# Optimization experiments

Hardware: AMD Instinct MI355X
Metric: run time of the kernel (lower is better)

The kernel has to match this reference:

```python
import jax, jax.numpy as jnp
import numpy as np

B, L, D = 64, 1024, 64  # (batch*heads, seq_len, head_dim)


def setup_inputs() -> dict:
    key = jax.random.key(0)
    kq, kk, kv = jax.random.split(key, 3)
    q = jax.random.normal(kq, (B, L, D), dtype=jnp.float32)
    k = jax.random.normal(kk, (B, L, D), dtype=jnp.float32)
    v = jax.random.normal(kv, (B, L, D), dtype=jnp.float32)
    scale = jnp.float32(1.0 / np.sqrt(D))  # standard 1/sqrt(d_head)
    return {"q": q, "k": k, "v": v, "scale": scale}


def reference(q, k, v, scale):
    # attention = bmm(q, k^T) * scale  -> [B, L, L]
    attention = jnp.einsum("bqd,bkd->bqk", q, k) * scale
    # softmax over dim=2 (keys); dropout p=0.0 is identity
    attention = jax.nn.softmax(attention, axis=2)
    # context = bmm(attention, v) -> [B, L, D]
    context = jnp.einsum("bqk,bkd->bqd", attention, v)
    return (context, attention)
```

## Files before the change

### kernel.cpp

```cpp
#include <hip/hip_runtime.h>
#include <hip/hip_bf16.h>

typedef __bf16 bf16x8 __attribute__((ext_vector_type(8)));
typedef float  f32x4  __attribute__((ext_vector_type(4)));

#define NB 64
#define LL 1024
#define DD 64
#define PSTR 36

#define LDS_K_BYTES (LL * DD * 2)
#define LDS_TOTAL   (LDS_K_BYTES + 8 * 16 * PSTR * 4)

__global__ __launch_bounds__(256)
void preconvert_v(const float* __restrict__ v, __bf16* __restrict__ vt) {
  const int blk = blockIdx.x, tid = threadIdx.x;
  const int b = blk >> 4, t = blk & 15;
  __shared__ float tile[64][65];
  const float* src = v + ((size_t)b * LL + t * 64) * DD;
  for (int i = tid; i < 64 * 16; i += 256) {
    const int row = i >> 4, c4 = (i & 15) * 4;
    f32x4 x = *(const f32x4*)(src + row * DD + c4);
    tile[row][c4 + 0] = x[0]; tile[row][c4 + 1] = x[1];
    tile[row][c4 + 2] = x[2]; tile[row][c4 + 3] = x[3];
  }
  __syncthreads();
  __bf16* dst = vt + (size_t)b * DD * LL + t * 64;
  for (int i = tid; i < 64 * 8; i += 256) {
    const int d = i >> 3, k8 = (i & 7) * 8;
    bf16x8 o;
    #pragma unroll
    for (int j = 0; j < 8; ++j) o[j] = (__bf16)tile[k8 + j][d];
    *(bf16x8*)(dst + (size_t)d * LL + k8) = o;
  }
}

__global__ __launch_bounds__(512, 1)
void sdpa_resident(const float* __restrict__ q, const float* __restrict__ kf,
                   const __bf16* __restrict__ vt, const float* __restrict__ scale_p,
                   float* __restrict__ out) {
  extern __shared__ char smem[];
  __bf16* Klds = (__bf16*)smem;
  float*  Pw   = (float*)(smem + LDS_K_BYTES);

  const int tid  = threadIdx.x;
  const int lane = tid & 63;
  const int w    = tid >> 6;
  const int l15  = lane & 15;
  const int lg   = lane >> 4;

  int bid = blockIdx.x;
  bid = (bid & 7) * 32 + (bid >> 3);
  const int b     = bid >> 2;
  const int qrow0 = (bid & 3) * 256 + w * 32;

  const float scale = scale_p[0];
  const float* kb = kf + (size_t)b * LL * DD;
  const __bf16* vb = vt + (size_t)b * DD * LL;
  float* ctxb  = out + ((size_t)b * LL + qrow0) * DD;
  float* attnb = out + (size_t)NB * LL * DD + (size_t)b * LL * LL
               + (size_t)qrow0 * LL;

  #pragma unroll
  for (int it = 0; it < 16; ++it) {
    const int c = it * 512 + tid;
    const int row = c >> 3, slot = c & 7;
    const f32x4* s4 = (const f32x4*)(kb + (size_t)c * 8);
    f32x4 x0 = s4[0], x1 = s4[1];
    bf16x8 t;
    #pragma unroll
    for (int j = 0; j < 4; ++j) { t[j] = (__bf16)x0[j]; t[4 + j] = (__bf16)x1[j]; }
    *(bf16x8*)(Klds + row * 64 + ((slot * 8) ^ ((row & 7) * 8))) = t;
  }

  bf16x8 aq[2][2];
  #pragma unroll
  for (int u = 0; u < 2; ++u) {
    const float* qrow = q + ((size_t)b * LL + qrow0 + u * 16 + l15) * DD;
    #pragma unroll
    for (int s = 0; s < 2; ++s) {
      const f32x4* p4 = (const f32x4*)(qrow + s * 32 + lg * 8);
      f32x4 x0 = p4[0], x1 = p4[1];
      #pragma unroll
      for (int j = 0; j < 4; ++j) {
        aq[u][s][j]     = (__bf16)(x0[j] * scale);
        aq[u][s][4 + j] = (__bf16)(x1[j] * scale);
      }
    }
  }

  __syncthreads();

  const int xsw = (l15 & 7) * 8;

  float lsum[2] = {0.f, 0.f};
  for (int kt = 0; kt < LL / 32; ++kt) {
    bf16x8 bk[2][2];
    #pragma unroll
    for (int f = 0; f < 2; ++f)
      #pragma unroll
      for (int s = 0; s < 2; ++s)
        bk[f][s] = *(const bf16x8*)(Klds + (kt * 32 + f * 16 + l15) * 64
                                         + ((s * 32 + lg * 8) ^ xsw));
    #pragma unroll
    for (int u = 0; u < 2; ++u) {
      f32x4 sacc[2] = {{0.f,0.f,0.f,0.f},{0.f,0.f,0.f,0.f}};
      #pragma unroll
      for (int s = 0; s < 2; ++s)
        #pragma unroll
        for (int f = 0; f < 2; ++f)
          sacc[f] = __builtin_amdgcn_mfma_f32_16x16x32_bf16(bk[f][s], aq[u][s], sacc[f], 0, 0, 0);
      #pragma unroll
      for (int f = 0; f < 2; ++f)
        #pragma unroll
        for (int r = 0; r < 4; ++r)
          lsum[u] += __expf(sacc[f][r]);
    }
  }
  #pragma unroll
  for (int u = 0; u < 2; ++u) {
    lsum[u] += __shfl_xor(lsum[u], 16, 64);
    lsum[u] += __shfl_xor(lsum[u], 32, 64);
  }
  const float rl[2] = {1.0f / lsum[0], 1.0f / lsum[1]};

  f32x4 cacc[2][4];
  #pragma unroll
  for (int u = 0; u < 2; ++u)
    #pragma unroll
    for (int g = 0; g < 4; ++g)
      cacc[u][g] = (f32x4){0.f, 0.f, 0.f, 0.f};

  float* prow = Pw + (w * 16 + l15) * PSTR;

  bf16x8 bvn[4];
  #pragma unroll
  for (int g = 0; g < 4; ++g)
    bvn[g] = *(const bf16x8*)(vb + (size_t)(g * 16 + l15) * LL + lg * 8);

  for (int kt = 0; kt < LL / 32; ++kt) {
    bf16x8 bvc[4];
    #pragma unroll
    for (int g = 0; g < 4; ++g) bvc[g] = bvn[g];
    if (kt + 1 < LL / 32) {
      #pragma unroll
      for (int g = 0; g < 4; ++g)
        bvn[g] = *(const bf16x8*)(vb + (size_t)(g * 16 + l15) * LL
                                     + (kt + 1) * 32 + lg * 8);
    }

    bf16x8 bk[2][2];
    #pragma unroll
    for (int f = 0; f < 2; ++f)
      #pragma unroll
      for (int s = 0; s < 2; ++s)
        bk[f][s] = *(const bf16x8*)(Klds + (kt * 32 + f * 16 + l15) * 64
                                         + ((s * 32 + lg * 8) ^ xsw));

    #pragma unroll
    for (int u = 0; u < 2; ++u) {
      f32x4 sacc[2] = {{0.f,0.f,0.f,0.f},{0.f,0.f,0.f,0.f}};
      #pragma unroll
      for (int s = 0; s < 2; ++s)
        #pragma unroll
        for (int f = 0; f < 2; ++f)
          sacc[f] = __builtin_amdgcn_mfma_f32_16x16x32_bf16(bk[f][s], aq[u][s], sacc[f], 0, 0, 0);

      f32x4 pv[2];
      #pragma unroll
      for (int f = 0; f < 2; ++f)
        #pragma unroll
        for (int r = 0; r < 4; ++r)
          pv[f][r] = __expf(sacc[f][r]) * rl[u];

      float* arow = attnb + (size_t)(u * 16 + l15) * LL + kt * 32 + lg * 4;
      *(f32x4*)(arow)      = pv[0];
      *(f32x4*)(arow + 16) = pv[1];

      *(f32x4*)(prow + lg * 4)      = pv[0];
      *(f32x4*)(prow + 16 + lg * 4) = pv[1];
      f32x4 p0 = *(const f32x4*)(prow + lg * 8);
      f32x4 p1 = *(const f32x4*)(prow + lg * 8 + 4);
      bf16x8 pa;
      #pragma unroll
      for (int j = 0; j < 4; ++j) { pa[j] = (__bf16)p0[j]; pa[4 + j] = (__bf16)p1[j]; }

      #pragma unroll
      for (int g = 0; g < 4; ++g)
        cacc[u][g] = __builtin_amdgcn_mfma_f32_16x16x32_bf16(pa, bvc[g], cacc[u][g], 0, 0, 0);
    }
  }

  #pragma unroll
  for (int u = 0; u < 2; ++u)
    #pragma unroll
    for (int g = 0; g < 4; ++g)
      #pragma unroll
      for (int r = 0; r < 4; ++r)
        ctxb[(size_t)(u * 16 + lg * 4 + r) * DD + g * 16 + l15] = cacc[u][g][r];
}

#define BQ 64
#define BK 32
#define KSTRIDE 72
#define VSTRIDE 40
#define PSTRIDE 48

__global__ __launch_bounds__(256, 4)
void sdpa_fallback(const float* __restrict__ q, const float* __restrict__ k,
                   const float* __restrict__ v, const float* __restrict__ scale_p,
                   float* __restrict__ out) {
  const int tid  = threadIdx.x;
  const int lane = tid & 63;
  const int w    = tid >> 6;
  int bid = blockIdx.x;
  bid = (bid & 7) * 128 + (bid >> 3);
  const int b    = bid >> 4;
  const int qblk = (bid & 15) * BQ;

  __shared__ __bf16 Ks[BK * KSTRIDE];
  __shared__ __bf16 Vs[DD * VSTRIDE];
  __shared__ __bf16 Pp[4][16 * PSTRIDE];

  const float scale = scale_p[0];
  const float* qb = q + ((size_t)b * LL + qblk) * DD;
  const float* kb = k + (size_t)b * LL * DD;
  const float* vb = v + (size_t)b * LL * DD;
  float* ctx  = out + ((size_t)b * LL + qblk) * DD;
  float* attn = out + (size_t)NB * LL * DD + (size_t)b * LL * LL + (size_t)qblk * LL;

  const int l15 = lane & 15;
  const int lg  = lane >> 4;
  const int dchunk = lg * 8;

  bf16x8 aq[2];
  {
    const float* qrow = qb + (size_t)(w * 16 + l15) * DD;
    #pragma unroll
    for (int s = 0; s < 2; ++s) {
      const f32x4* p4 = (const f32x4*)(qrow + s * 32 + dchunk);
      f32x4 x0 = p4[0], x1 = p4[1];
      #pragma unroll
      for (int j = 0; j < 4; ++j) {
        aq[s][j]     = (__bf16)(x0[j] * scale);
        aq[s][4 + j] = (__bf16)(x1[j] * scale);
      }
    }
  }

  const int srow = tid >> 3;
  const int sd0  = (tid & 7) * 8;

  float lpart[4] = {0.f, 0.f, 0.f, 0.f};
  for (int kt = 0; kt < LL / BK; ++kt) {
    __syncthreads();
    {
      const f32x4* src = (const f32x4*)(kb + (size_t)(kt * BK + srow) * DD + sd0);
      f32x4 x0 = src[0], x1 = src[1];
      bf16x8 t;
      #pragma unroll
      for (int j = 0; j < 4; ++j) { t[j] = (__bf16)x0[j]; t[4 + j] = (__bf16)x1[j]; }
      *(bf16x8*)&Ks[srow * KSTRIDE + sd0] = t;
    }
    __syncthreads();
    f32x4 sacc[2] = {{0.f,0.f,0.f,0.f},{0.f,0.f,0.f,0.f}};
    #pragma unroll
    for (int s = 0; s < 2; ++s)
      #pragma unroll
      for (int f = 0; f < 2; ++f) {
        bf16x8 bk = *(const bf16x8*)&Ks[(f * 16 + l15) * KSTRIDE + s * 32 + dchunk];
        sacc[f] = __builtin_amdgcn_mfma_f32_16x16x32_bf16(aq[s], bk, sacc[f], 0, 0, 0);
      }
    #pragma unroll
    for (int f = 0; f < 2; ++f)
      #pragma unroll
      for (int r = 0; r < 4; ++r)
        lpart[r] += __expf(sacc[f][r]);
  }
  #pragma unroll
  for (int m = 1; m < 16; m <<= 1)
    #pragma unroll
    for (int r = 0; r < 4; ++r)
      lpart[r] += __shfl_xor(lpart[r], m, 64);
  float rl[4];
  #pragma unroll
  for (int r = 0; r < 4; ++r) rl[r] = 1.0f / lpart[r];

  f32x4 cacc[4] = {{0.f,0.f,0.f,0.f},{0.f,0.f,0.f,0.f},
                   {0.f,0.f,0.f,0.f},{0.f,0.f,0.f,0.f}};
  for (int kt = 0; kt < LL / BK; ++kt) {
    __syncthreads();
    {
      const f32x4* src = (const f32x4*)(kb + (size_t)(kt * BK + srow) * DD + sd0);
      f32x4 x0 = src[0], x1 = src[1];
      bf16x8 t;
      #pragma unroll
      for (int j = 0; j < 4; ++j) { t[j] = (__bf16)x0[j]; t[4 + j] = (__bf16)x1[j]; }
      *(bf16x8*)&Ks[srow * KSTRIDE + sd0] = t;
      const f32x4* vsrc = (const f32x4*)(vb + (size_t)(kt * BK + srow) * DD + sd0);
      f32x4 y0 = vsrc[0], y1 = vsrc[1];
      #pragma unroll
      for (int j = 0; j < 4; ++j) {
        Vs[(sd0 + j)     * VSTRIDE + srow] = (__bf16)y0[j];
        Vs[(sd0 + 4 + j) * VSTRIDE + srow] = (__bf16)y1[j];
      }
    }
    __syncthreads();
    f32x4 sacc[2] = {{0.f,0.f,0.f,0.f},{0.f,0.f,0.f,0.f}};
    #pragma unroll
    for (int s = 0; s < 2; ++s)
      #pragma unroll
      for (int f = 0; f < 2; ++f) {
        bf16x8 bk = *(const bf16x8*)&Ks[(f * 16 + l15) * KSTRIDE + s * 32 + dchunk];
        sacc[f] = __builtin_amdgcn_mfma_f32_16x16x32_bf16(aq[s], bk, sacc[f], 0, 0, 0);
      }
    #pragma unroll
    for (int f = 0; f < 2; ++f)
      #pragma unroll
      for (int r = 0; r < 4; ++r) {
        const int row = lg * 4 + r;
        float p = __expf(sacc[f][r]) * rl[r];
        attn[(size_t)(w * 16 + row) * LL + (kt * BK + f * 16 + l15)] = p;
        Pp[w][row * PSTRIDE + f * 16 + l15] = (__bf16)p;
      }
    bf16x8 pa = *(const bf16x8*)&Pp[w][l15 * PSTRIDE + lg * 8];
    #pragma unroll
    for (int g = 0; g < 4; ++g) {
      bf16x8 bv = *(const bf16x8*)&Vs[(g * 16 + l15) * VSTRIDE + lg * 8];
      cacc[g] = __builtin_amdgcn_mfma_f32_16x16x32_bf16(pa, bv, cacc[g], 0, 0, 0);
    }
  }
  #pragma unroll
  for (int g = 0; g < 4; ++g)
    #pragma unroll
    for (int r = 0; r < 4; ++r)
      ctx[(size_t)(w * 16 + lg * 4 + r) * DD + g * 16 + l15] = cacc[g][r];
}

extern "C" void kernel_launch(void* const* d_in, const int* in_sizes, int n_in,
                              void* d_out, int out_size, void* d_ws, size_t ws_size,
                              hipStream_t stream) {
  const float* q = (const float*)d_in[0];
  const float* k = (const float*)d_in[1];
  const float* v = (const float*)d_in[2];
  const float* s = (const float*)d_in[3];
  float* out = (float*)d_out;

  const size_t vbytes = (size_t)NB * LL * DD * 2;
  if (ws_size >= vbytes) {
    __bf16* vt = (__bf16*)d_ws;
    preconvert_v<<<dim3(NB * (LL / 64)), dim3(256), 0, stream>>>(v, vt);
    (void)hipFuncSetAttribute((const void*)sdpa_resident,
                              hipFuncAttributeMaxDynamicSharedMemorySize,
                              LDS_TOTAL);
    sdpa_resident<<<dim3(256), dim3(512), LDS_TOTAL, stream>>>(q, k, vt, s, out);
  } else {
    sdpa_fallback<<<dim3(NB * (LL / 64)), dim3(256), 0, stream>>>(q, k, v, s, out);
  }
}
```

Baseline: 109.7 us.

## Split row-sum pass into own kernel; stage K/V halves in LDS and coalesce attention stores

The single resident kernel becomes two kernels. The first computes softmax row sums and writes reciprocals to the workspace. The second stages K and pre-transposed V in LDS in two halves of 512 keys, uses exp2 with a folded log2e scale, and re-reads P from LDS so each attention row segment is written with wider, row-contiguous stores. This targets uncoalesced attention-matrix writes and the per-iteration global V loads. In exchange it adds a kernel launch, recomputes QK^T plus a K reload in the second kernel, and requires a larger workspace.

```diff
diff --git a/kernel.cpp b/kernel.cpp
--- a/kernel.cpp
+++ b/kernel.cpp
@@ -7,10 +7,21 @@
 #define NB 64
 #define LL 1024
 #define DD 64
+#define HK 512
 #define PSTR 36
 
-#define LDS_K_BYTES (LL * DD * 2)
-#define LDS_TOTAL   (LDS_K_BYTES + 8 * 16 * PSTR * 4)
+#define LSUM_LDS  (LL * DD * 2)
+#define MAIN_LDS  (2 * HK * DD * 2 + 8 * 16 * PSTR * 4)
+
+#define WS_VT_OFF 0
+#define WS_RL_OFF ((size_t)8 * 1024 * 1024)
+#define WS_NEED   (WS_RL_OFF + (size_t)NB * LL * 4)
+
+#if __has_builtin(__builtin_amdgcn_exp2f)
+#define EXP2(x) __builtin_amdgcn_exp2f(x)
+#else
+#define EXP2(x) exp2f(x)
+#endif
 
 __global__ __launch_bounds__(256)
 void preconvert_v(const float* __restrict__ v, __bf16* __restrict__ vt) {
@@ -36,12 +47,10 @@
 }
 
 __global__ __launch_bounds__(512, 1)
-void sdpa_resident(const float* __restrict__ q, const float* __restrict__ kf,
-                   const __bf16* __restrict__ vt, const float* __restrict__ scale_p,
-                   float* __restrict__ out) {
+void lsum_kernel(const float* __restrict__ q, const float* __restrict__ kf,
+                 const float* __restrict__ scale_p, float* __restrict__ rlbuf) {
   extern __shared__ char smem[];
   __bf16* Klds = (__bf16*)smem;
-  float*  Pw   = (float*)(smem + LDS_K_BYTES);
 
   const int tid  = threadIdx.x;
   const int lane = tid & 63;
@@ -54,12 +63,8 @@
   const int b     = bid >> 2;
   const int qrow0 = (bid & 3) * 256 + w * 32;
 
-  const float scale = scale_p[0];
+  const float scale2 = scale_p[0] * 1.4426950408889634f;
   const float* kb = kf + (size_t)b * LL * DD;
-  const __bf16* vb = vt + (size_t)b * DD * LL;
-  float* ctxb  = out + ((size_t)b * LL + qrow0) * DD;
-  float* attnb = out + (size_t)NB * LL * DD + (size_t)b * LL * LL
-               + (size_t)qrow0 * LL;
 
   #pragma unroll
   for (int it = 0; it < 16; ++it) {
@@ -83,8 +88,8 @@
       f32x4 x0 = p4[0], x1 = p4[1];
       #pragma unroll
       for (int j = 0; j < 4; ++j) {
-        aq[u][s][j]     = (__bf16)(x0[j] * scale);
-        aq[u][s][4 + j] = (__bf16)(x1[j] * scale);
+        aq[u][s][j]     = (__bf16)(x0[j] * scale2);
+        aq[u][s][4 + j] = (__bf16)(x1[j] * scale2);
       }
     }
   }
@@ -92,9 +97,8 @@
   __syncthreads();
 
   const int xsw = (l15 & 7) * 8;
-
-  float lsum[2] = {0.f, 0.f};
-  for (int kt = 0; kt < LL / 32; ++kt) {
+  float ls[2] = {0.f, 0.f};
+  for (int kt = 0; kt < 32; ++kt) {
     bf16x8 bk[2][2];
     #pragma unroll
     for (int f = 0; f < 2; ++f)
@@ -114,15 +118,71 @@
       for (int f = 0; f < 2; ++f)
         #pragma unroll
         for (int r = 0; r < 4; ++r)
-          lsum[u] += __expf(sacc[f][r]);
+          ls[u] += EXP2(sacc[f][r]);
     }
   }
   #pragma unroll
   for (int u = 0; u < 2; ++u) {
-    lsum[u] += __shfl_xor(lsum[u], 16, 64);
-    lsum[u] += __shfl_xor(lsum[u], 32, 64);
-  }
-  const float rl[2] = {1.0f / lsum[0], 1.0f / lsum[1]};
+    ls[u] += __shfl_xor(ls[u], 16, 64);
+    ls[u] += __shfl_xor(ls[u], 32, 64);
+  }
+  if (lg == 0) {
+    float* rp = rlbuf + (size_t)b * LL + qrow0 + l15;
+    rp[0]  = 1.0f / ls[0];
+    rp[16] = 1.0f / ls[1];
+  }
+}
+
+__global__ __launch_bounds__(512, 1)
+void sdpa_store(const float* __restrict__ q, const float* __restrict__ kf,
+                const __bf16* __restrict__ vt, const float* __restrict__ rlbuf,
+                const float* __restrict__ scale_p, float* __restrict__ out) {
+  extern __shared__ char smem[];
+  __bf16* Klds = (__bf16*)smem;
+  __bf16* Vlds = (__bf16*)(smem + HK * DD * 2);
+  float*  Pw   = (float*)(smem + 2 * HK * DD * 2);
+
+  const int tid  = threadIdx.x;
+  const int lane = tid & 63;
+  const int w    = tid >> 6;
+  const int l15  = lane & 15;
+  const int lg   = lane >> 4;
+
+  int bid = blockIdx.x;
+  bid = (bid & 7) * 32 + (bid >> 3);
+  const int b     = bid >> 2;
+  const int qrow0 = (bid & 3) * 256 + w * 32;
+
+  const float scale2 = scale_p[0] * 1.4426950408889634f;
+  const float* kb  = kf + (size_t)b * LL * DD;
+  const __bf16* vb = vt + (size_t)b * DD * LL;
+  float* ctxb  = out + ((size_t)b * LL + qrow0) * DD;
+  float* attnb = out + (size_t)NB * LL * DD + (size_t)b * LL * LL
+               + (size_t)qrow0 * LL;
+
+  bf16x8 aq[2][2];
+  #pragma unroll
+  for (int u = 0; u < 2; ++u) {
+    const float* qrow = q + ((size_t)b * LL + qrow0 + u * 16 + l15) * DD;
+    #pragma unroll
+    for (int s = 0; s < 2; ++s) {
+      const f32x4* p4 = (const f32x4*)(qrow + s * 32 + lg * 8);
+      f32x4 x0 = p4[0], x1 = p4[1];
+      #pragma unroll
+      for (int j = 0; j < 4; ++j) {
+        aq[u][s][j]     = (__bf16)(x0[j] * scale2);
+        aq[u][s][4 + j] = (__bf16)(x1[j] * scale2);
+      }
+    }
+  }
+  const float* rlp = rlbuf + (size_t)b * LL + qrow0 + l15;
+  const float rl[2] = {rlp[0], rlp[16]};
+
+  const int xsw = (l15 & 7) * 8;
+  float* prow  = Pw + (w * 16 + l15) * PSTR;
+  const int srl = lane >> 3;
+  const int src8 = (lane & 7) * 4;
+  const float* psr = Pw + (w * 16) * PSTR;
 
   f32x4 cacc[2][4];
   #pragma unroll
@@ -131,63 +191,74 @@
     for (int g = 0; g < 4; ++g)
       cacc[u][g] = (f32x4){0.f, 0.f, 0.f, 0.f};
 
-  float* prow = Pw + (w * 16 + l15) * PSTR;
-
-  bf16x8 bvn[4];
-  #pragma unroll
-  for (int g = 0; g < 4; ++g)
-    bvn[g] = *(const bf16x8*)(vb + (size_t)(g * 16 + l15) * LL + lg * 8);
-
-  for (int kt = 0; kt < LL / 32; ++kt) {
-    bf16x8 bvc[4];
-    #pragma unroll
-    for (int g = 0; g < 4; ++g) bvc[g] = bvn[g];
-    if (kt + 1 < LL / 32) {
+  for (int h = 0; h < 2; ++h) {
+    __syncthreads();
+    #pragma unroll
+    for (int it = 0; it < 8; ++it) {
+      const int c = it * 512 + tid;
+      const int row = c >> 3, slot = c & 7;
+      const f32x4* s4 = (const f32x4*)(kb + ((size_t)(h * HK + row) * DD) + slot * 8);
+      f32x4 x0 = s4[0], x1 = s4[1];
+      bf16x8 t;
+      #pragma unroll
+      for (int j = 0; j < 4; ++j) { t[j] = (__bf16)x0[j]; t[4 + j] = (__bf16)x1[j]; }
+      *(bf16x8*)(Klds + row * 64 + ((slot * 8) ^ ((row & 7) * 8))) = t;
+
+      const int d = c >> 6, ks = c & 63;
+      bf16x8 tv = *(const bf16x8*)(vb + (size_t)d * LL + h * HK + ks * 8);
+      *(bf16x8*)(Vlds + d * HK + ((ks * 8) ^ ((d & 7) * 8))) = tv;
+    }
+    __syncthreads();
+
+    for (int kt = 0; kt < HK / 32; ++kt) {
+      bf16x8 bk[2][2];
+      #pragma unroll
+      for (int f = 0; f < 2; ++f)
+        #pragma unroll
+        for (int s = 0; s < 2; ++s)
+          bk[f][s] = *(const bf16x8*)(Klds + (kt * 32 + f * 16 + l15) * 64
+                                           + ((s * 32 + lg * 8) ^ xsw));
+      bf16x8 bv[4];
       #pragma unroll
       for (int g = 0; g < 4; ++g)
-        bvn[g] = *(const bf16x8*)(vb + (size_t)(g * 16 + l15) * LL
-                                     + (kt + 1) * 32 + lg * 8);
-    }
-
-    bf16x8 bk[2][2];
-    #pragma unroll
-    for (int f = 0; f < 2; ++f)
-      #pragma unroll
-      for (int s = 0; s < 2; ++s)
-        bk[f][s] = *(const bf16x8*)(Klds + (kt * 32 + f * 16 + l15) * 64
-                                         + ((s * 32 + lg * 8) ^ xsw));
-
-    #pragma unroll
-    for (int u = 0; u < 2; ++u) {
-      f32x4 sacc[2] = {{0.f,0.f,0.f,0.f},{0.f,0.f,0.f,0.f}};
-      #pragma unroll
-      for (int s = 0; s < 2; ++s)
-        #pragma unroll
-        for (int f = 0; f < 2; ++f)
-          sacc[f] = __builtin_amdgcn_mfma_f32_16x16x32_bf16(bk[f][s], aq[u][s], sacc[f], 0, 0, 0);
-
-      f32x4 pv[2];
-      #pragma unroll
-      for (int f = 0; f < 2; ++f)
-        #pragma unroll
-        for (int r = 0; r < 4; ++r)
-          pv[f][r] = __expf(sacc[f][r]) * rl[u];
-
-      float* arow = attnb + (size_t)(u * 16 + l15) * LL + kt * 32 + lg * 4;
-      *(f32x4*)(arow)      = pv[0];
-      *(f32x4*)(arow + 16) = pv[1];
-
-      *(f32x4*)(prow + lg * 4)      = pv[0];
-      *(f32x4*)(prow + 16 + lg * 4) = pv[1];
-      f32x4 p0 = *(const f32x4*)(prow + lg * 8);
-      f32x4 p1 = *(const f32x4*)(prow + lg * 8 + 4);
-      bf16x8 pa;
-      #pragma unroll
-      for (int j = 0; j < 4; ++j) { pa[j] = (__bf16)p0[j]; pa[4 + j] = (__bf16)p1[j]; }
-
-      #pragma unroll
-      for (int g = 0; g < 4; ++g)
-        cacc[u][g] = __builtin_amdgcn_mfma_f32_16x16x32_bf16(pa, bvc[g], cacc[u][g], 0, 0, 0);
+        bv[g] = *(const bf16x8*)(Vlds + (g * 16 + l15) * HK
+                                      + ((kt * 32 + lg * 8) ^ xsw));
+
+      #pragma unroll
+      for (int u = 0; u < 2; ++u) {
+        f32x4 sacc[2] = {{0.f,0.f,0.f,0.f},{0.f,0.f,0.f,0.f}};
+        #pragma unroll
+        for (int s = 0; s < 2; ++s)
+          #pragma unroll
+          for (int f = 0; f < 2; ++f)
+            sacc[f] = __builtin_amdgcn_mfma_f32_16x16x32_bf16(bk[f][s], aq[u][s], sacc[f], 0, 0, 0);
+
+        #pragma unroll
+        for (int f = 0; f < 2; ++f) {
+          f32x4 pv;
+          #pragma unroll
+          for (int r = 0; r < 4; ++r)
+            pv[r] = EXP2(sacc[f][r]) * rl[u];
+          *(f32x4*)(prow + f * 16 + lg * 4) = pv;
+        }
+
+        f32x4 p0 = *(const f32x4*)(prow + lg * 8);
+        f32x4 p1 = *(const f32x4*)(prow + lg * 8 + 4);
+        bf16x8 pa;
+        #pragma unroll
+        for (int j = 0; j < 4; ++j) { pa[j] = (__bf16)p0[j]; pa[4 + j] = (__bf16)p1[j]; }
+        #pragma unroll
+        for (int g = 0; g < 4; ++g)
+          cacc[u][g] = __builtin_amdgcn_mfma_f32_16x16x32_bf16(pa, bv[g], cacc[u][g], 0, 0, 0);
+
+        #pragma unroll
+        for (int j = 0; j < 2; ++j) {
+          const int srow = j * 8 + srl;
+          f32x4 sp = *(const f32x4*)(psr + srow * PSTR + src8);
+          *(f32x4*)(attnb + (size_t)(u * 16 + srow) * LL
+                          + h * HK + kt * 32 + src8) = sp;
+        }
+      }
     }
   }
 
@@ -346,14 +417,16 @@
   const float* s = (const float*)d_in[3];
   float* out = (float*)d_out;
 
-  const size_t vbytes = (size_t)NB * LL * DD * 2;
-  if (ws_size >= vbytes) {
-    __bf16* vt = (__bf16*)d_ws;
+  if (ws_size >= WS_NEED) {
+    __bf16* vt = (__bf16*)((char*)d_ws + WS_VT_OFF);
+    float*  rl = (float*)((char*)d_ws + WS_RL_OFF);
     preconvert_v<<<dim3(NB * (LL / 64)), dim3(256), 0, stream>>>(v, vt);
-    (void)hipFuncSetAttribute((const void*)sdpa_resident,
-                              hipFuncAttributeMaxDynamicSharedMemorySize,
-                              LDS_TOTAL);
-    sdpa_resident<<<dim3(256), dim3(512), LDS_TOTAL, stream>>>(q, k, vt, s, out);
+    (void)hipFuncSetAttribute((const void*)lsum_kernel,
+                              hipFuncAttributeMaxDynamicSharedMemorySize, LSUM_LDS);
+    lsum_kernel<<<dim3(256), dim3(512), LSUM_LDS, stream>>>(q, k, s, rl);
+    (void)hipFuncSetAttribute((const void*)sdpa_store,
+                              hipFuncAttributeMaxDynamicSharedMemorySize, MAIN_LDS);
+    sdpa_store<<<dim3(256), dim3(512), MAIN_LDS, stream>>>(q, k, vt, rl, s, out);
   } else {
     sdpa_fallback<<<dim3(NB * (LL / 64)), dim3(256), 0, stream>>>(q, k, v, s, out);
   }
```

After: 107.8 us. Within noise of the previous version (-1.7%).
